# Kernel optimization log

Hardware: AMD Instinct MI355X
Metric: run time of the kernel (lower is better)

The kernel has to match this reference:

```python
import jax, jax.numpy as jnp
import numpy as np

B, T, INPUT, H, NCLS = 16384, 64, 78, 8, 11

def setup_inputs() -> dict:
    key = jax.random.key(0)
    ks = jax.random.split(key, 9)
    s = lambda fan: 1.0 / np.sqrt(fan)
    return {
        "x":   jax.random.normal(ks[0], (B, T, INPUT), dtype=jnp.float32),
        "W_ih": jax.random.normal(ks[1], (4 * H, INPUT), dtype=jnp.float32) * s(H),
        "W_hh": jax.random.normal(ks[2], (4 * H, H), dtype=jnp.float32) * s(H),
        "b_ih": jax.random.normal(ks[3], (4 * H,), dtype=jnp.float32) * s(H),
        "b_hh": jax.random.normal(ks[4], (4 * H,), dtype=jnp.float32) * s(H),
        "W1":  jax.random.normal(ks[5], (16, H), dtype=jnp.float32) * s(H),
        "b1":  jax.random.normal(ks[6], (16,), dtype=jnp.float32) * s(H),
        "W2":  jax.random.normal(ks[7], (NCLS, 16), dtype=jnp.float32) * s(16),
        "b2":  jax.random.normal(ks[8], (NCLS,), dtype=jnp.float32) * s(16),
    }

def _lstm_last(x, W_ih, W_hh, b_ih, b_hh):
    # x: [B, T, INPUT]; PyTorch gate order i, f, g, o along the 4H axis.
    Bsz = x.shape[0]
    Hd = W_hh.shape[1]
    # Precompute input projections for all timesteps: [T, B, 4H]
    xg = jnp.einsum('bti,gi->tbg', x, W_ih) + (b_ih + b_hh)
    h0 = jnp.zeros((Bsz, Hd), dtype=x.dtype)
    c0 = jnp.zeros((Bsz, Hd), dtype=x.dtype)

    def step(carry, xg_t):
        h, c = carry
        gates = xg_t + h @ W_hh.T  # [B, 4H]
        i, f, g, o = jnp.split(gates, 4, axis=-1)
        i = jax.nn.sigmoid(i)
        f = jax.nn.sigmoid(f)
        g = jnp.tanh(g)
        o = jax.nn.sigmoid(o)
        c = f * c + i * g
        h = o * jnp.tanh(c)
        return (h, c), None

    (h, _), _ = jax.lax.scan(step, (h0, c0), xg)
    return h  # last hidden state == out[:, -1, :]

def reference(x, W_ih, W_hh, b_ih, b_hh, W1, b1, W2, b2):
    h = _lstm_last(x, W_ih, W_hh, b_ih, b_hh)      # [B, H]
    # dropout is identity in eval mode
    h = jax.nn.relu(h)
    h = h @ W1.T + b1                               # [B, 16]
    h = jax.nn.relu(h)
    h = h @ W2.T + b2                               # [B, num_classes]
    return jax.nn.softmax(h, axis=-1)
```

## Files before the change

### kernel.cpp

```cpp
#include <hip/hip_runtime.h>


typedef float v2f __attribute__((ext_vector_type(2)));

#define B_SZ 16384
#define T_SZ 64
#define IN_SZ 78
#define H_SZ 8
#define NCLS 11
#define NB 16
#define TT 4
#define NTHREADS 256
#define NITER (T_SZ / TT)
#define ROWSTR (T_SZ * IN_SZ)
#define ROWF (TT * IN_SZ)
#define TILE_F4 (NB * ROWF / 4)
#define TILE_F4_PAD 1280

__device__ __forceinline__ float sigm(float x) { return 1.0f / (1.0f + __expf(-x)); }

template<int CTRL>
__device__ __forceinline__ float dpp_f(float x) {
    return __int_as_float(__builtin_amdgcn_update_dpp(
        0, __float_as_int(x), CTRL, 0xF, 0xF, true));
}
template<int CTRL>
__device__ __forceinline__ v2f dpp2(v2f v) {
    v2f r; r.x = dpp_f<CTRL>(v.x); r.y = dpp_f<CTRL>(v.y); return r;
}

__global__ __launch_bounds__(NTHREADS, 4)
void lstm_fused(const float* __restrict__ x,
                const float* __restrict__ W_ih,
                const float* __restrict__ W_hh,
                const float* __restrict__ b_ih,
                const float* __restrict__ b_hh,
                const float* __restrict__ W1,
                const float* __restrict__ b1,
                const float* __restrict__ W2,
                const float* __restrict__ b2,
                float* __restrict__ out)
{
    __shared__ float x2f[TILE_F4_PAD * 4];
    __shared__ float Wq[39 * 16 * 4];
    __shared__ float z1s[NB][17];

    const int tid  = threadIdx.x;
    const int type = tid & 3;
    const int pr   = (tid >> 2) & 3;
    const int rr   = tid >> 4;
    const int u    = tid & 15;
    const bool isT = (type == 2);

    const size_t rowbase = (size_t)blockIdx.x * NB;
    const float* xb = x + rowbase * ROWSTR;
    const float4* xb4 = (const float4*)xb;

    const int G0 = type * 8 + 2 * pr;
    const int G1 = G0 + 1;
    v2f bias; bias.x = b_ih[G0] + b_hh[G0]; bias.y = b_ih[G1] + b_hh[G1];
    float4 WhhP[4];
    #pragma unroll
    for (int m = 0; m < 4; ++m) {
        int p = pr ^ m;
        WhhP[m].x = W_hh[G0 * H_SZ + 2 * p];
        WhhP[m].y = W_hh[G0 * H_SZ + 2 * p + 1];
        WhhP[m].z = W_hh[G1 * H_SZ + 2 * p];
        WhhP[m].w = W_hh[G1 * H_SZ + 2 * p + 1];
    }

    int og[5];
    {
        int r0 = tid / IN_SZ;
        int q  = tid - r0 * IN_SZ;
        int oo = r0 * 1248 + q;
        #pragma unroll
        for (int j = 0; j < 5; ++j) {
            og[j] = oo;
            q += 22; oo += 3766;
            if (q >= IN_SZ) { q -= IN_SZ; oo += 1170; }
        }
        if (tid >= 224) og[4] = og[3];
    }

    float4 xv[5];
    #pragma unroll
    for (int j = 0; j < 5; ++j) xv[j] = xb4[og[j]];

    for (int i = tid; i < 39 * 64; i += NTHREADS) {
        int e = i & 3, gl = (i >> 2) & 15, kp = i >> 6;
        int ty = gl & 3, pp = gl >> 2;
        int G = ty * 8 + 2 * pp + (e >> 1);
        int k = 2 * kp + (e & 1);
        Wq[i] = W_ih[G * IN_SZ + k];
    }

    float4* x2_4 = (float4*)x2f;
    #pragma unroll
    for (int j = 0; j < 5; ++j) x2_4[tid + j * NTHREADS] = xv[j];
    __syncthreads();

    v2f c2; c2.x = 0.f; c2.y = 0.f;
    v2f hrot[4];
    #pragma unroll
    for (int m = 0; m < 4; ++m) { hrot[m].x = 0.f; hrot[m].y = 0.f; }

    const v2f*    x2v = (const v2f*)x2f;
    const float4* wq4 = (const float4*)Wq;
    float accx[TT], accy[TT];

    #pragma unroll
    for (int tt = 0; tt < TT; ++tt) { accx[tt] = bias.x; accy[tt] = bias.y; }
    #pragma unroll 3
    for (int kp = 0; kp < 39; ++kp) {
        float4 wv = wq4[kp * 16 + u];
        #pragma unroll
        for (int tt = 0; tt < TT; ++tt) {
            v2f xk = x2v[rr * 156 + tt * 39 + kp];
            accx[tt] = fmaf(xk.x, wv.x, accx[tt]);
            accx[tt] = fmaf(xk.y, wv.y, accx[tt]);
            accy[tt] = fmaf(xk.x, wv.z, accy[tt]);
            accy[tt] = fmaf(xk.y, wv.w, accy[tt]);
        }
    }

    auto lstm_step = [&](float vx, float vy) {
        #pragma unroll
        for (int m = 0; m < 4; ++m) {
            vx = fmaf(hrot[m].x, WhhP[m].x, vx);
            vx = fmaf(hrot[m].y, WhhP[m].y, vx);
            vy = fmaf(hrot[m].x, WhhP[m].z, vy);
            vy = fmaf(hrot[m].y, WhhP[m].w, vy);
        }
        v2f a;
        {
            float ax = isT ? 2.0f * vx : vx;
            float ay = isT ? 2.0f * vy : vy;
            float sx = sigm(ax), sy = sigm(ay);
            a.x = isT ? 2.0f * sx - 1.0f : sx;
            a.y = isT ? 2.0f * sy - 1.0f : sy;
        }
        v2f i2 = dpp2<0x00>(a);
        v2f f2 = dpp2<0x55>(a);
        v2f g2 = dpp2<0xAA>(a);
        v2f o2 = dpp2<0xFF>(a);
        c2.x = fmaf(f2.x, c2.x, i2.x * g2.x);
        c2.y = fmaf(f2.y, c2.y, i2.y * g2.y);
        v2f th;
        th.x = 2.0f * sigm(2.0f * c2.x) - 1.0f;
        th.y = 2.0f * sigm(2.0f * c2.y) - 1.0f;
        v2f h2; h2.x = o2.x * th.x; h2.y = o2.y * th.y;
        hrot[0] = h2;
        hrot[1] = dpp2<0x141>(h2);
        hrot[2] = dpp2<0x128>(h2);
        hrot[3] = dpp2<0x140>(h2);
    };

    for (int it = 1; it < NITER; ++it) {
        const float4* xit4 = xb4 + it * 78;
        #pragma unroll
        for (int j = 0; j < 5; ++j) xv[j] = xit4[og[j]];

        #pragma unroll
        for (int tt = 0; tt < TT; ++tt) lstm_step(accx[tt], accy[tt]);

        __syncthreads();
        #pragma unroll
        for (int j = 0; j < 5; ++j) x2_4[tid + j * NTHREADS] = xv[j];
        __syncthreads();

        #pragma unroll
        for (int tt = 0; tt < TT; ++tt) { accx[tt] = bias.x; accy[tt] = bias.y; }
        #pragma unroll 3
        for (int kp = 0; kp < 39; ++kp) {
            float4 wv = wq4[kp * 16 + u];
            #pragma unroll
            for (int tt = 0; tt < TT; ++tt) {
                v2f xk = x2v[rr * 156 + tt * 39 + kp];
                accx[tt] = fmaf(xk.x, wv.x, accx[tt]);
                accx[tt] = fmaf(xk.y, wv.y, accx[tt]);
                accy[tt] = fmaf(xk.x, wv.z, accy[tt]);
                accy[tt] = fmaf(xk.y, wv.w, accy[tt]);
            }
        }
    }
    #pragma unroll
    for (int tt = 0; tt < TT; ++tt) lstm_step(accx[tt], accy[tt]);

    {
        float z1 = b1[u];
        #pragma unroll
        for (int m = 0; m < 4; ++m) {
            int p = pr ^ m;
            z1 += fmaxf(hrot[m].x, 0.0f) * W1[u * H_SZ + 2 * p];
            z1 += fmaxf(hrot[m].y, 0.0f) * W1[u * H_SZ + 2 * p + 1];
        }
        z1s[rr][u] = fmaxf(z1, 0.0f);
    }
    __syncthreads();
    if (tid < NB) {
        const int row = tid;
        float z1v[16];
        #pragma unroll
        for (int uu = 0; uu < 16; ++uu) z1v[uu] = z1s[row][uu];
        float z2[NCLS];
        float m = -1e30f;
        #pragma unroll
        for (int c = 0; c < NCLS; ++c) {
            float v = b2[c];
            #pragma unroll
            for (int uu = 0; uu < 16; ++uu) v += z1v[uu] * W2[c * 16 + uu];
            z2[c] = v;
            m = fmaxf(m, v);
        }
        float s = 0.0f;
        #pragma unroll
        for (int c = 0; c < NCLS; ++c) { z2[c] = __expf(z2[c] - m); s += z2[c]; }
        float inv = 1.0f / s;
        float* op = out + (rowbase + row) * NCLS;
        #pragma unroll
        for (int c = 0; c < NCLS; ++c) op[c] = z2[c] * inv;
    }
}

extern "C" void kernel_launch(void* const* d_in, const int* in_sizes, int n_in,
                              void* d_out, int out_size, void* d_ws, size_t ws_size,
                              hipStream_t stream) {
    const float* x    = (const float*)d_in[0];
    const float* W_ih = (const float*)d_in[1];
    const float* W_hh = (const float*)d_in[2];
    const float* b_ih = (const float*)d_in[3];
    const float* b_hh = (const float*)d_in[4];
    const float* W1   = (const float*)d_in[5];
    const float* b1   = (const float*)d_in[6];
    const float* W2   = (const float*)d_in[7];
    const float* b2   = (const float*)d_in[8];
    float* outp = (float*)d_out;

    lstm_fused<<<dim3(B_SZ / NB), dim3(NTHREADS), 0, stream>>>(
        x, W_ih, W_hh, b_ih, b_hh, W1, b1, W2, b2, outp);
}
```

Measured before the change: 530.3 us.

## Double-buffer x tiles via direct global-to-LDS loads and prepack weights in workspace

Input tiles now go straight from global memory into one of two LDS buffers using global_load_lds. The next chunk's load is issued before computing the current chunk, which removes the register staging and one barrier per iteration. A small prep kernel packs W_ih, W_hh and the summed biases into the workspace. The main kernel then reads W_ih from global/L2 instead of LDS, which frees LDS but may add latency to the projection loop. The relies on correct LDS placement of the wave-level DMA, and the extra launch adds a little overhead.

Result: no change. 521.1 us (-1.7%).

```diff
diff --git a/kernel.cpp b/kernel.cpp
--- a/kernel.cpp
+++ b/kernel.cpp
@@ -13,9 +13,12 @@
 #define NTHREADS 256
 #define NITER (T_SZ / TT)
 #define ROWSTR (T_SZ * IN_SZ)
-#define ROWF (TT * IN_SZ)
-#define TILE_F4 (NB * ROWF / 4)
+#define TILE_F4 1248
 #define TILE_F4_PAD 1280
+
+#define WS_WQ   0
+#define WS_WHH  2496
+#define WS_BIAS 2752
 
 __device__ __forceinline__ float sigm(float x) { return 1.0f / (1.0f + __expf(-x)); }
 
@@ -29,21 +32,54 @@
     v2f r; r.x = dpp_f<CTRL>(v.x); r.y = dpp_f<CTRL>(v.y); return r;
 }
 
+__device__ __forceinline__ void dma16(const float4* g, float4* l) {
+    __builtin_amdgcn_global_load_lds(
+        (const __attribute__((address_space(1))) void*)g,
+        (__attribute__((address_space(3))) void*)l,
+        16, 0, 0);
+}
+
+__global__ __launch_bounds__(NTHREADS)
+void prep_kernel(const float* __restrict__ W_ih,
+                 const float* __restrict__ W_hh,
+                 const float* __restrict__ b_ih,
+                 const float* __restrict__ b_hh,
+                 float* __restrict__ ws)
+{
+    const int tid = threadIdx.x;
+    for (int i = tid; i < 39 * 16 * 4; i += NTHREADS) {
+        int e = i & 3, u = (i >> 2) & 15, kp = i >> 6;
+        int ty = u & 3, pp = u >> 2;
+        int G = ty * 8 + 2 * pp + (e >> 1);
+        int k = 2 * kp + (e & 1);
+        ws[WS_WQ + i] = W_ih[G * IN_SZ + k];
+    }
+    for (int i = tid; i < 16 * 4 * 4; i += NTHREADS) {
+        int e = i & 3, m = (i >> 2) & 3, u = i >> 4;
+        int ty = u & 3, pp = u >> 2;
+        int p = pp ^ m;
+        int G = ty * 8 + 2 * pp + (e >> 1);
+        int j = 2 * p + (e & 1);
+        ws[WS_WHH + i] = W_hh[G * H_SZ + j];
+    }
+    if (tid < 32) {
+        int e = tid & 1, u = tid >> 1;
+        int ty = u & 3, pp = u >> 2;
+        int G = ty * 8 + 2 * pp + e;
+        ws[WS_BIAS + tid] = b_ih[G] + b_hh[G];
+    }
+}
+
 __global__ __launch_bounds__(NTHREADS, 4)
 void lstm_fused(const float* __restrict__ x,
-                const float* __restrict__ W_ih,
-                const float* __restrict__ W_hh,
-                const float* __restrict__ b_ih,
-                const float* __restrict__ b_hh,
+                const float* __restrict__ ws,
                 const float* __restrict__ W1,
                 const float* __restrict__ b1,
                 const float* __restrict__ W2,
                 const float* __restrict__ b2,
                 float* __restrict__ out)
 {
-    __shared__ float x2f[TILE_F4_PAD * 4];
-    __shared__ float Wq[39 * 16 * 4];
-    __shared__ float z1s[NB][17];
+    __shared__ float4 xbuf[2][TILE_F4_PAD];
 
     const int tid  = threadIdx.x;
     const int type = tid & 3;
@@ -53,21 +89,14 @@
     const bool isT = (type == 2);
 
     const size_t rowbase = (size_t)blockIdx.x * NB;
-    const float* xb = x + rowbase * ROWSTR;
-    const float4* xb4 = (const float4*)xb;
-
-    const int G0 = type * 8 + 2 * pr;
-    const int G1 = G0 + 1;
-    v2f bias; bias.x = b_ih[G0] + b_hh[G0]; bias.y = b_ih[G1] + b_hh[G1];
+    const float4* xb4 = (const float4*)(x + rowbase * ROWSTR);
+
+    v2f bias = *(const v2f*)&ws[WS_BIAS + 2 * u];
     float4 WhhP[4];
     #pragma unroll
-    for (int m = 0; m < 4; ++m) {
-        int p = pr ^ m;
-        WhhP[m].x = W_hh[G0 * H_SZ + 2 * p];
-        WhhP[m].y = W_hh[G0 * H_SZ + 2 * p + 1];
-        WhhP[m].z = W_hh[G1 * H_SZ + 2 * p];
-        WhhP[m].w = W_hh[G1 * H_SZ + 2 * p + 1];
-    }
+    for (int m = 0; m < 4; ++m)
+        WhhP[m] = *(const float4*)&ws[WS_WHH + u * 16 + m * 4];
+    const float4* wq4 = (const float4*)&ws[WS_WQ];
 
     int og[5];
     {
@@ -82,22 +111,11 @@
         }
         if (tid >= 224) og[4] = og[3];
     }
-
-    float4 xv[5];
-    #pragma unroll
-    for (int j = 0; j < 5; ++j) xv[j] = xb4[og[j]];
-
-    for (int i = tid; i < 39 * 64; i += NTHREADS) {
-        int e = i & 3, gl = (i >> 2) & 15, kp = i >> 6;
-        int ty = gl & 3, pp = gl >> 2;
-        int G = ty * 8 + 2 * pp + (e >> 1);
-        int k = 2 * kp + (e & 1);
-        Wq[i] = W_ih[G * IN_SZ + k];
-    }
-
-    float4* x2_4 = (float4*)x2f;
-    #pragma unroll
-    for (int j = 0; j < 5; ++j) x2_4[tid + j * NTHREADS] = xv[j];
+    const int wavebase = tid & 192;
+
+    #pragma unroll
+    for (int j = 0; j < 5; ++j)
+        dma16(xb4 + og[j], &xbuf[0][j * NTHREADS + wavebase]);
     __syncthreads();
 
     v2f c2; c2.x = 0.f; c2.y = 0.f;
@@ -105,24 +123,24 @@
     #pragma unroll
     for (int m = 0; m < 4; ++m) { hrot[m].x = 0.f; hrot[m].y = 0.f; }
 
-    const v2f*    x2v = (const v2f*)x2f;
-    const float4* wq4 = (const float4*)Wq;
     float accx[TT], accy[TT];
 
-    #pragma unroll
-    for (int tt = 0; tt < TT; ++tt) { accx[tt] = bias.x; accy[tt] = bias.y; }
-    #pragma unroll 3
-    for (int kp = 0; kp < 39; ++kp) {
-        float4 wv = wq4[kp * 16 + u];
-        #pragma unroll
-        for (int tt = 0; tt < TT; ++tt) {
-            v2f xk = x2v[rr * 156 + tt * 39 + kp];
-            accx[tt] = fmaf(xk.x, wv.x, accx[tt]);
-            accx[tt] = fmaf(xk.y, wv.y, accx[tt]);
-            accy[tt] = fmaf(xk.x, wv.z, accy[tt]);
-            accy[tt] = fmaf(xk.y, wv.w, accy[tt]);
-        }
-    }
+    auto do_proj = [&](const v2f* xtv) {
+        #pragma unroll
+        for (int tt = 0; tt < TT; ++tt) { accx[tt] = bias.x; accy[tt] = bias.y; }
+        #pragma unroll 3
+        for (int kp = 0; kp < 39; ++kp) {
+            float4 wv = wq4[kp * 16 + u];
+            #pragma unroll
+            for (int tt = 0; tt < TT; ++tt) {
+                v2f xk = xtv[rr * 156 + tt * 39 + kp];
+                accx[tt] = fmaf(xk.x, wv.x, accx[tt]);
+                accx[tt] = fmaf(xk.y, wv.y, accx[tt]);
+                accy[tt] = fmaf(xk.x, wv.z, accy[tt]);
+                accy[tt] = fmaf(xk.y, wv.w, accy[tt]);
+            }
+        }
+    };
 
     auto lstm_step = [&](float vx, float vy) {
         #pragma unroll
@@ -156,37 +174,24 @@
         hrot[3] = dpp2<0x140>(h2);
     };
 
-    for (int it = 1; it < NITER; ++it) {
-        const float4* xit4 = xb4 + it * 78;
-        #pragma unroll
-        for (int j = 0; j < 5; ++j) xv[j] = xit4[og[j]];
-
+    for (int t = 0; t < NITER - 1; ++t) {
+        const float4* xsrc = xb4 + (t + 1) * 78;
+        float4* dbuf = xbuf[(t + 1) & 1];
+        #pragma unroll
+        for (int j = 0; j < 5; ++j)
+            dma16(xsrc + og[j], &dbuf[j * NTHREADS + wavebase]);
+
+        do_proj((const v2f*)xbuf[t & 1]);
         #pragma unroll
         for (int tt = 0; tt < TT; ++tt) lstm_step(accx[tt], accy[tt]);
 
         __syncthreads();
-        #pragma unroll
-        for (int j = 0; j < 5; ++j) x2_4[tid + j * NTHREADS] = xv[j];
-        __syncthreads();
-
-        #pragma unroll
-        for (int tt = 0; tt < TT; ++tt) { accx[tt] = bias.x; accy[tt] = bias.y; }
-        #pragma unroll 3
-        for (int kp = 0; kp < 39; ++kp) {
-            float4 wv = wq4[kp * 16 + u];
-            #pragma unroll
-            for (int tt = 0; tt < TT; ++tt) {
-                v2f xk = x2v[rr * 156 + tt * 39 + kp];
-                accx[tt] = fmaf(xk.x, wv.x, accx[tt]);
-                accx[tt] = fmaf(xk.y, wv.y, accx[tt]);
-                accy[tt] = fmaf(xk.x, wv.z, accy[tt]);
-                accy[tt] = fmaf(xk.y, wv.w, accy[tt]);
-            }
-        }
-    }
+    }
+    do_proj((const v2f*)xbuf[(NITER - 1) & 1]);
     #pragma unroll
     for (int tt = 0; tt < TT; ++tt) lstm_step(accx[tt], accy[tt]);
 
+    float* z1f = (float*)&xbuf[0][0];
     {
         float z1 = b1[u];
         #pragma unroll
@@ -195,14 +200,14 @@
             z1 += fmaxf(hrot[m].x, 0.0f) * W1[u * H_SZ + 2 * p];
             z1 += fmaxf(hrot[m].y, 0.0f) * W1[u * H_SZ + 2 * p + 1];
         }
-        z1s[rr][u] = fmaxf(z1, 0.0f);
+        z1f[rr * 17 + u] = fmaxf(z1, 0.0f);
     }
     __syncthreads();
     if (tid < NB) {
         const int row = tid;
         float z1v[16];
         #pragma unroll
-        for (int uu = 0; uu < 16; ++uu) z1v[uu] = z1s[row][uu];
+        for (int uu = 0; uu < 16; ++uu) z1v[uu] = z1f[row * 17 + uu];
         float z2[NCLS];
         float m = -1e30f;
         #pragma unroll
@@ -236,7 +241,9 @@
     const float* W2   = (const float*)d_in[7];
     const float* b2   = (const float*)d_in[8];
     float* outp = (float*)d_out;
-
+    float* ws   = (float*)d_ws;
+
+    prep_kernel<<<dim3(1), dim3(NTHREADS), 0, stream>>>(W_ih, W_hh, b_ih, b_hh, ws);
     lstm_fused<<<dim3(B_SZ / NB), dim3(NTHREADS), 0, stream>>>(
-        x, W_ih, W_hh, b_ih, b_hh, W1, b1, W2, b2, outp);
-}
+        x, ws, W1, b1, W2, b2, outp);
+}
```
